# Optimization experiments

Hardware: AMD Instinct MI355X
Metric: run time of the kernel (lower is better)

Reference implementation:

```python
import jax, jax.numpy as jnp
import numpy as np

EPS = 1e-8

def _qparams(x, bits):
    # AsymmetricSignedQParams + GlobalMinMaxObserver: per-tensor min/max,
    # signed range [-2^(b-1), 2^(b-1)-1], asymmetric zero point.
    qmin = -(2 ** (bits - 1))
    qmax = 2 ** (bits - 1) - 1
    mn = jnp.minimum(jnp.min(x), 0.0)
    mx = jnp.maximum(jnp.max(x), 0.0)
    scale = jnp.maximum((mx - mn) / (qmax - qmin), EPS)
    zp = jnp.clip(jnp.round(qmin - mn / scale), qmin, qmax)
    return scale, zp, qmin, qmax

def _fake_quant(x, bits):
    # quantize -> clamp -> dequantize (simulated fixed-point as in float forward)
    scale, zp, qmin, qmax = _qparams(x, bits)
    q = jnp.clip(jnp.round(x / scale) + zp, qmin, qmax)
    return (q - zp) * scale


def setup_inputs() -> dict:
    key = jax.random.key(0)
    k1, k2, k3 = jax.random.split(key, 3)
    B, W, H, D = 8, 1024, 8, 64
    q = jax.random.normal(k1, (B, W, H, D), dtype=jnp.float32)
    k = jax.random.normal(k2, (B, W, H, D), dtype=jnp.float32)
    v = jax.random.normal(k3, (B, W, H, D), dtype=jnp.float32)
    return {"q": q, "k": k, "v": v, "quant_bits": 8}


def reference(q, k, v, quant_bits):
    bits = int(quant_bits)
    d_model = q.shape[-1]
    inv_sqrt_d = 1.0 / np.sqrt(d_model)

    # quantize-dequantize inputs (inputs_{q,k,v}_QParams)
    qf = _fake_quant(q, bits)
    kf = _fake_quant(k, bits)
    vf = _fake_quant(v, bits)

    # matrix_multi_score: quantized QK^T with folded 1/sqrt(d) scale,
    # then requantize output (matrix_multi_score.outputs_QParams)
    scores = jnp.einsum("bqhd,bkhd->bhqk", qf, kf) * inv_sqrt_d
    scores = _fake_quant(scores, bits)

    # SoftmaxLUT: softmax over last dim, result requantized (softmax.outputs_QParams)
    att = jax.nn.softmax(scores, axis=-1)
    att_q = _fake_quant(att, bits)

    # matrix_multi_att: quantized att @ V, requantized output
    context = jnp.einsum("bhqk,bkhd->bqhd", att_q, vf)
    context = _fake_quant(context, bits)

    return context, att_q
```

## Files before the change

kernel.cpp:

```cpp
#include <hip/hip_runtime.h>
#include <cstdint>
#include <cstddef>

#define W  1024
#define NH 8
#define NB 8
#define DH 64
#define BHN (NB*NH)
#define CTX_ELEMS ((size_t)NB*W*NH*DH)
#define NS 64
#define ROWF 512

typedef int v4i __attribute__((ext_vector_type(4)));


__device__ __forceinline__ unsigned enc_f(float f){
  unsigned u = __float_as_uint(f);
  return (u & 0x80000000u) ? ~u : (u | 0x80000000u);
}
__device__ __forceinline__ float dec_f(unsigned k){
  unsigned u = (k & 0x80000000u) ? (k ^ 0x80000000u) : ~k;
  return __uint_as_float(u);
}

__device__ __forceinline__ float fq1(float x, float s, float z, float mn, float mx){
  float t = rintf(x / s) + z;
  t = fminf(fmaxf(t, mn), mx);
  return (t - z) * s;
}
__device__ __forceinline__ int qint_m(float x, float is, float z, float mn, float mx){
  return (int)fminf(fmaxf(rintf(x * is) + z, mn), mx);
}
__device__ __forceinline__ unsigned pack4(int a0, int a1, int a2, int a3){
  return (unsigned)(a0 & 0xff) | ((unsigned)(a1 & 0xff) << 8) |
         ((unsigned)(a2 & 0xff) << 16) | ((unsigned)(a3 & 0xff) << 24);
}

__device__ __forceinline__ unsigned* slot_min(unsigned* s, int t){ return s + (size_t)(2*t)*NS; }
__device__ __forceinline__ unsigned* slot_max(unsigned* s, int t){ return s + (size_t)(2*t+1)*NS; }

__device__ __forceinline__ void blk_minmax_atomic(float lmin, float lmax,
                                                  unsigned* smin, unsigned* smax){
  #pragma unroll
  for (int o = 32; o; o >>= 1){
    lmin = fminf(lmin, __shfl_xor(lmin, o));
    lmax = fmaxf(lmax, __shfl_xor(lmax, o));
  }
  __shared__ float wmn[4], wmx[4];
  int wid = threadIdx.x >> 6, lane = threadIdx.x & 63;
  if (lane == 0){ wmn[wid] = lmin; wmx[wid] = lmax; }
  __syncthreads();
  if (threadIdx.x == 0){
    float a = wmn[0], b = wmx[0];
    for (int w = 1; w < (int)(blockDim.x >> 6); ++w){
      a = fminf(a, wmn[w]); b = fmaxf(b, wmx[w]);
    }
    atomicMin(smin, enc_f(a));
    atomicMax(smax, enc_f(b));
  }
}

__device__ __forceinline__ void blk_iminmax_atomic(int lmin, int lmax, int* gmin, int* gmax){
  #pragma unroll
  for (int o = 32; o; o >>= 1){
    lmin = min(lmin, __shfl_xor(lmin, o));
    lmax = max(lmax, __shfl_xor(lmax, o));
  }
  __shared__ int iwmn[4], iwmx[4];
  int wid = threadIdx.x >> 6, lane = threadIdx.x & 63;
  if (lane == 0){ iwmn[wid] = lmin; iwmx[wid] = lmax; }
  __syncthreads();
  if (threadIdx.x == 0){
    int a = iwmn[0], b = iwmx[0];
    for (int w = 1; w < (int)(blockDim.x >> 6); ++w){
      a = min(a, iwmn[w]); b = max(b, iwmx[w]);
    }
    atomicMin(gmin, a);
    atomicMax(gmax, b);
  }
}

__device__ __forceinline__ void stage_tile(const float* __restrict__ rowptr,
                                           signed char (*S)[80], int* __restrict__ Ssum,
                                           float is, float z, float mn, float mx, int t){
  const int rr = t >> 2, dq = (t & 3) << 4;
  const float* p = rowptr + (size_t)rr * ROWF + dq;
  int part = 0;
  #pragma unroll
  for (int g = 0; g < 4; ++g){
    float4 x = *(const float4*)(p + g * 4);
    int a0 = qint_m(x.x, is, z, mn, mx), a1 = qint_m(x.y, is, z, mn, mx);
    int a2 = qint_m(x.z, is, z, mn, mx), a3 = qint_m(x.w, is, z, mn, mx);
    part += a0 + a1 + a2 + a3;
    *(unsigned*)&S[rr][dq + g*4] = pack4(a0, a1, a2, a3);
  }
  int x1 = part + __shfl_xor(part, 1);
  int tot = x1 + __shfl_xor(x1, 2);
  if ((t & 3) == 0) Ssum[rr] = tot;
}


__global__ void init_slots_kernel(unsigned* __restrict__ slots, int* __restrict__ jmn,
                                  int* __restrict__ jmx){
  for (int i = threadIdx.x; i < 6*2*NS; i += blockDim.x)
    slots[i] = 0x80000000u;
  if (threadIdx.x < NS){
    jmn[threadIdx.x] = 0x7fffffff;
    jmx[threadIdx.x] = (int)0x80000000;
  }
}

__global__ __launch_bounds__(256) void minmax3_kernel(const float* __restrict__ q,
                                                      const float* __restrict__ k,
                                                      const float* __restrict__ v,
                                                      unsigned* __restrict__ slots){
  const float4* p = (const float4*)(blockIdx.y == 0 ? q : (blockIdx.y == 1 ? k : v));
  float lmin = 0.f, lmax = 0.f;
  const int n4 = (int)(CTX_ELEMS / 4);
  for (int i = blockIdx.x * blockDim.x + threadIdx.x; i < n4; i += gridDim.x * blockDim.x){
    float4 x = p[i];
    lmin = fminf(lmin, fminf(fminf(x.x, x.y), fminf(x.z, x.w)));
    lmax = fmaxf(lmax, fmaxf(fmaxf(x.x, x.y), fmaxf(x.z, x.w)));
  }
  const int idx = blockIdx.x & (NS - 1);
  blk_minmax_atomic(lmin, lmax, slot_min(slots, blockIdx.y) + idx, slot_max(slots, blockIdx.y) + idx);
}

__global__ void finalize_kernel(unsigned* __restrict__ slots, int* __restrict__ jmn,
                                int* __restrict__ jmx, float* __restrict__ params,
                                const int* __restrict__ bits_p, int t0, int t1){
  if (threadIdx.x == 0 && blockIdx.x == 0){
    int bits = *bits_p;
    float qmn = -(float)(1 << (bits - 1));
    float qmx = (float)((1 << (bits - 1)) - 1);
    for (int t = t0; t < t1; ++t){
      float mn, mx;
      if (t == 3){
        int em = jmn[0], ex = jmx[0];
        for (int i = 1; i < NS; ++i){ em = min(em, jmn[i]); ex = max(ex, jmx[i]); }
        float cfac = 0.125f * (params[0] * params[4]);
        mn = fminf(cfac * (float)em, 0.0f);
        mx = fmaxf(cfac * (float)ex, 0.0f);
      } else {
        unsigned* pm = slot_min(slots, t);
        unsigned* px = slot_max(slots, t);
        unsigned em = pm[0], ex = px[0];
        for (int i = 1; i < NS; ++i){
          em = (pm[i] < em) ? pm[i] : em;
          ex = (px[i] > ex) ? px[i] : ex;
        }
        mn = dec_f(em); mx = dec_f(ex);
      }
      float sc = fmaxf((mx - mn) / (qmx - qmn), 1e-8f);
      float zp = fminf(fmaxf(rintf(qmn - mn / sc), qmn), qmx);
      params[4*t + 0] = sc; params[4*t + 1] = zp;
      params[4*t + 2] = qmn; params[4*t + 3] = qmx;
    }
  }
}

__global__ __launch_bounds__(256) void pass1_kernel(const float* __restrict__ qg,
                                                    const float* __restrict__ kg,
                                                    const float* __restrict__ params,
                                                    float* __restrict__ stash,
                                                    int* __restrict__ jmn,
                                                    int* __restrict__ jmx){
  __shared__ __align__(16) signed char Qs[64][80], Ks[64][80];
  __shared__ int Sq[64], Sk[64];
  const int it = blockIdx.x, bh = blockIdx.y, b = bh >> 3, h = bh & 7;
  const int i0 = it << 6, t = threadIdx.x;
  const int lane = t & 63, w = t >> 6, lr = lane & 15, lg = lane >> 4;
  const float sq = params[0], zq = params[1], qmn = params[2], qmx = params[3];
  const float sk = params[4], zk = params[5];
  const float isq = 1.0f / sq, isk = 1.0f / sk;
  const int izq = (int)zq, izk = (int)zk, c64 = 64 * izq * izk;

  stage_tile(qg + ((size_t)(b*W + i0) * NH + h) * DH, Qs, Sq, isq, zq, qmn, qmx, t);
  __syncthreads();
  const v4i Bq = *(const v4i*)&Qs[(w << 4) + lr][lg << 4];
  const int sqi = Sq[(w << 4) + lr];

  int gmin = 0x7fffffff, gmax = (int)0x80000000, rmax = (int)0x80000000;
  for (int cc = 0; cc < 16; ++cc){
    __syncthreads();
    stage_tile(kg + ((size_t)(b*W + (cc << 6)) * NH + h) * DH, Ks, Sk, isk, zk, qmn, qmx, t);
    __syncthreads();
    #pragma unroll
    for (int jt = 0; jt < 4; ++jt){
      v4i Ak = *(const v4i*)&Ks[(jt << 4) + lr][lg << 4];
      v4i zz = {0, 0, 0, 0};
      v4i acc = __builtin_amdgcn_mfma_i32_16x16x64_i8(Ak, Bq, zz, 0, 0, 0);
      v4i s4 = *(const v4i*)&Sk[(jt << 4) + (lg << 2)];
      #pragma unroll
      for (int r = 0; r < 4; ++r){
        int J = acc[r] - izq * s4[r] - izk * sqi + c64;
        gmin = min(gmin, J); gmax = max(gmax, J); rmax = max(rmax, J);
      }
    }
  }
  rmax = max(rmax, __shfl_xor(rmax, 16));
  rmax = max(rmax, __shfl_xor(rmax, 32));
  if (lg == 0)
    stash[((size_t)(b*W + i0 + (w << 4) + lr) * NH + h) * DH] = __int_as_float(rmax);
  const int idx = (it + bh * 16) & (NS - 1);
  blk_iminmax_atomic(gmin, gmax, jmn + idx, jmx + idx);
}

__global__ __launch_bounds__(256) void pass2_kernel(const float* __restrict__ qg,
                                                    const float* __restrict__ kg,
                                                    const float* __restrict__ params,
                                                    float* __restrict__ stash,
                                                    unsigned* __restrict__ slots){
  __shared__ __align__(16) signed char Qs[64][80], Ks[64][80];
  __shared__ int Sq[64], Sk[64];
  const int it = blockIdx.x, bh = blockIdx.y, b = bh >> 3, h = bh & 7;
  const int i0 = it << 6, t = threadIdx.x;
  const int lane = t & 63, w = t >> 6, lr = lane & 15, lg = lane >> 4;
  const float sq = params[0], zq = params[1], qmn = params[2], qmx = params[3];
  const float sk = params[4], zk = params[5];
  const float ss = params[12], zs = params[13], smn = params[14], smx = params[15];
  const float isq = 1.0f / sq, isk = 1.0f / sk;
  const int izq = (int)zq, izk = (int)zk, c64 = 64 * izq * izk;
  const float rf = (0.125f * (sq * sk)) / ss;
  const float c2 = ss * 1.4426950408889634f;

  stage_tile(qg + ((size_t)(b*W + i0) * NH + h) * DH, Qs, Sq, isq, zq, qmn, qmx, t);
  __syncthreads();
  const v4i Bq = *(const v4i*)&Qs[(w << 4) + lr][lg << 4];
  const int sqi = Sq[(w << 4) + lr];
  const int irow = (w << 4) + lr;
  int Jm = __float_as_int(stash[((size_t)(b*W + i0 + irow) * NH + h) * DH]);
  const float tmxf = fminf(fmaxf(rintf((float)Jm * rf) + zs, smn), smx);

  float zacc = 0.f;
  for (int cc = 0; cc < 16; ++cc){
    __syncthreads();
    stage_tile(kg + ((size_t)(b*W + (cc << 6)) * NH + h) * DH, Ks, Sk, isk, zk, qmn, qmx, t);
    __syncthreads();
    #pragma unroll
    for (int jt = 0; jt < 4; ++jt){
      v4i Ak = *(const v4i*)&Ks[(jt << 4) + lr][lg << 4];
      v4i zz = {0, 0, 0, 0};
      v4i acc = __builtin_amdgcn_mfma_i32_16x16x64_i8(Ak, Bq, zz, 0, 0, 0);
      v4i s4 = *(const v4i*)&Sk[(jt << 4) + (lg << 2)];
      #pragma unroll
      for (int r = 0; r < 4; ++r){
        int J = acc[r] - izq * s4[r] - izk * sqi + c64;
        float tl = fminf(fmaxf(rintf((float)J * rf) + zs, smn), smx);
        zacc += exp2f((tl - tmxf) * c2);
      }
    }
  }
  zacc += __shfl_xor(zacc, 16);
  zacc += __shfl_xor(zacc, 32);
  if (lg == 0)
    stash[((size_t)(b*W + i0 + irow) * NH + h) * DH + 1] = zacc;
  float ratt = 1.0f / zacc;
  #pragma unroll
  for (int o = 1; o < 16; o <<= 1) ratt = fmaxf(ratt, __shfl_xor(ratt, o));
  if (lane == 0){
    const int idx = ((it << 2) + w + bh * 64) & (NS - 1);
    atomicMax(slot_max(slots, 4) + idx, enc_f(ratt));
  }
}

__global__ __launch_bounds__(256) void pass3_kernel(const float* __restrict__ qg,
                                                    const float* __restrict__ kg,
                                                    const float* __restrict__ vg,
                                                    const float* __restrict__ params,
                                                    float* __restrict__ att,
                                                    float* __restrict__ ctx,
                                                    unsigned* __restrict__ slots){
  __shared__ __align__(16) signed char Qs[64][80], Ks[64][80], Vs[64][80], As[64][80];
  __shared__ int Sq[64], Sk[64];
  __shared__ int RowA[64], ColV[64];
  const int it = blockIdx.x, bh = blockIdx.y, b = bh >> 3, h = bh & 7;
  const int i0 = it << 6, t = threadIdx.x;
  const int lane = t & 63, w = t >> 6, lr = lane & 15, lg = lane >> 4;
  const float sq = params[0], zq = params[1], qmn = params[2], qmx = params[3];
  const float sk = params[4], zk = params[5];
  const float sv = params[8], zv = params[9], vmn = params[10], vmx = params[11];
  const float ss = params[12], zs = params[13], smn = params[14], smx = params[15];
  const float sa = params[16], za = params[17], amn = params[18], amx = params[19];
  const float isq = 1.0f / sq, isk = 1.0f / sk, isv = 1.0f / sv;
  const int izq = (int)zq, izk = (int)zk, c64 = 64 * izq * izk;
  const int iza = (int)za, izv = (int)zv;
  const float rf = (0.125f * (sq * sk)) / ss;
  const float c2 = ss * 1.4426950408889634f;
  const float inv_sa = 1.0f / sa;

  if (t < 64) ColV[t] = 0;
  stage_tile(qg + ((size_t)(b*W + i0) * NH + h) * DH, Qs, Sq, isq, zq, qmn, qmx, t);
  __syncthreads();
  const v4i Bq = *(const v4i*)&Qs[(w << 4) + lr][lg << 4];
  const int sqi = Sq[(w << 4) + lr];
  const int irow = (w << 4) + lr;
  const size_t rbase = ((size_t)(b*W + i0 + irow) * NH + h) * DH;
  int Jm = __float_as_int(ctx[rbase]);
  const float tmxf = fminf(fmaxf(rintf((float)Jm * rf) + zs, smn), smx);
  const float iZ = 1.0f / ctx[rbase + 1];

  const int dq4 = (t & 15) << 2;
  const int kb  = (t >> 4) << 2;
  int cv4[4] = {0, 0, 0, 0};
  int rA = 0;
  v4i accPV[4];
  #pragma unroll
  for (int tj = 0; tj < 4; ++tj){ v4i zz = {0,0,0,0}; accPV[tj] = zz; }

  for (int cc = 0; cc < 16; ++cc){
    __syncthreads();
    stage_tile(kg + ((size_t)(b*W + (cc << 6)) * NH + h) * DH, Ks, Sk, isk, zk, qmn, qmx, t);
    {
      const float* vp = vg + ((size_t)(b*W + (cc << 6) + kb) * NH + h) * DH + dq4;
      float4 x0 = *(const float4*)(vp);
      float4 x1 = *(const float4*)(vp + ROWF);
      float4 x2 = *(const float4*)(vp + 2 * ROWF);
      float4 x3 = *(const float4*)(vp + 3 * ROWF);
      int q00 = qint_m(x0.x, isv, zv, vmn, vmx), q01 = qint_m(x0.y, isv, zv, vmn, vmx),
          q02 = qint_m(x0.z, isv, zv, vmn, vmx), q03 = qint_m(x0.w, isv, zv, vmn, vmx);
      int q10 = qint_m(x1.x, isv, zv, vmn, vmx), q11 = qint_m(x1.y, isv, zv, vmn, vmx),
          q12 = qint_m(x1.z, isv, zv, vmn, vmx), q13 = qint_m(x1.w, isv, zv, vmn, vmx);
      int q20 = qint_m(x2.x, isv, zv, vmn, vmx), q21 = qint_m(x2.y, isv, zv, vmn, vmx),
          q22 = qint_m(x2.z, isv, zv, vmn, vmx), q23 = qint_m(x2.w, isv, zv, vmn, vmx);
      int q30 = qint_m(x3.x, isv, zv, vmn, vmx), q31 = qint_m(x3.y, isv, zv, vmn, vmx),
          q32 = qint_m(x3.z, isv, zv, vmn, vmx), q33 = qint_m(x3.w, isv, zv, vmn, vmx);
      cv4[0] += q00 + q10 + q20 + q30;
      cv4[1] += q01 + q11 + q21 + q31;
      cv4[2] += q02 + q12 + q22 + q32;
      cv4[3] += q03 + q13 + q23 + q33;
      *(unsigned*)&Vs[dq4 + 0][kb] = pack4(q00, q10, q20, q30);
      *(unsigned*)&Vs[dq4 + 1][kb] = pack4(q01, q11, q21, q31);
      *(unsigned*)&Vs[dq4 + 2][kb] = pack4(q02, q12, q22, q32);
      *(unsigned*)&Vs[dq4 + 3][kb] = pack4(q03, q13, q23, q33);
    }
    __syncthreads();
    #pragma unroll
    for (int jt = 0; jt < 4; ++jt){
      v4i Ak = *(const v4i*)&Ks[(jt << 4) + lr][lg << 4];
      v4i zz = {0, 0, 0, 0};
      v4i acc = __builtin_amdgcn_mfma_i32_16x16x64_i8(Ak, Bq, zz, 0, 0, 0);
      v4i s4 = *(const v4i*)&Sk[(jt << 4) + (lg << 2)];
      float4 y;
      int J0 = acc[0] - izq * s4[0] - izk * sqi + c64;
      int J1 = acc[1] - izq * s4[1] - izk * sqi + c64;
      int J2 = acc[2] - izq * s4[2] - izk * sqi + c64;
      int J3 = acc[3] - izq * s4[3] - izk * sqi + c64;
      float tl0 = fminf(fmaxf(rintf((float)J0 * rf) + zs, smn), smx);
      float tl1 = fminf(fmaxf(rintf((float)J1 * rf) + zs, smn), smx);
      float tl2 = fminf(fmaxf(rintf((float)J2 * rf) + zs, smn), smx);
      float tl3 = fminf(fmaxf(rintf((float)J3 * rf) + zs, smn), smx);
      float p0 = exp2f((tl0 - tmxf) * c2) * iZ;
      float p1 = exp2f((tl1 - tmxf) * c2) * iZ;
      float p2 = exp2f((tl2 - tmxf) * c2) * iZ;
      float p3 = exp2f((tl3 - tmxf) * c2) * iZ;
      float a0 = fminf(fmaxf(rintf(p0 * inv_sa) + za, amn), amx);
      float a1 = fminf(fmaxf(rintf(p1 * inv_sa) + za, amn), amx);
      float a2 = fminf(fmaxf(rintf(p2 * inv_sa) + za, amn), amx);
      float a3 = fminf(fmaxf(rintf(p3 * inv_sa) + za, amn), amx);
      y.x = (a0 - za) * sa; y.y = (a1 - za) * sa;
      y.z = (a2 - za) * sa; y.w = (a3 - za) * sa;
      *(float4*)(att + ((size_t)bh << 20) + (size_t)(i0 + irow) * W
                 + (cc << 6) + (jt << 4) + (lg << 2)) = y;
      int q0 = (int)a0, q1 = (int)a1, q2 = (int)a2, q3 = (int)a3;
      rA += q0 + q1 + q2 + q3;
      *(unsigned*)&As[irow][(jt << 4) + (lg << 2)] = pack4(q0, q1, q2, q3);
    }
    __syncthreads();
    {
      v4i A2 = *(const v4i*)&As[(w << 4) + lr][lg << 4];
      #pragma unroll
      for (int tj = 0; tj < 4; ++tj){
        v4i B2 = *(const v4i*)&Vs[(tj << 4) + lr][lg << 4];
        accPV[tj] = __builtin_amdgcn_mfma_i32_16x16x64_i8(A2, B2, accPV[tj], 0, 0, 0);
      }
    }
  }

  rA += __shfl_xor(rA, 16);
  rA += __shfl_xor(rA, 32);
  if (lg == 0) RowA[irow] = rA;
  #pragma unroll
  for (int j = 0; j < 4; ++j) atomicAdd(&ColV[dq4 + j], cv4[j]);
  __syncthreads();

  const float sav = sa * sv;
  float lmin = 0.f, lmax = 0.f;
  #pragma unroll
  for (int tj = 0; tj < 4; ++tj){
    const int d = (tj << 4) + lr;
    #pragma unroll
    for (int r = 0; r < 4; ++r){
      const int i = (w << 4) + (lg << 2) + r;
      int Jv = accPV[tj][r] - iza * ColV[d] - izv * RowA[i] + 1024 * iza * izv;
      float c = sav * (float)Jv;
      lmin = fminf(lmin, c); lmax = fmaxf(lmax, c);
      ctx[(((size_t)(b * W + i0 + i)) * NH + h) * DH + d] = c;
    }
  }
  const int idx = (it + bh * 16) & (NS - 1);
  blk_minmax_atomic(lmin, lmax, slot_min(slots, 5) + idx, slot_max(slots, 5) + idx);
}

__global__ __launch_bounds__(256) void quantctx_kernel(float* __restrict__ ctx,
                                                       const float* __restrict__ params){
  const float s = params[20], z = params[21], mn = params[22], mx = params[23];
  size_t i = (size_t)blockIdx.x * blockDim.x + threadIdx.x;
  float4* p = (float4*)ctx;
  float4 x = p[i];
  x.x = fq1(x.x, s, z, mn, mx);
  x.y = fq1(x.y, s, z, mn, mx);
  x.z = fq1(x.z, s, z, mn, mx);
  x.w = fq1(x.w, s, z, mn, mx);
  p[i] = x;
}


extern "C" void kernel_launch(void* const* d_in, const int* in_sizes, int n_in,
                              void* d_out, int out_size, void* d_ws, size_t ws_size,
                              hipStream_t stream){
  const float* q = (const float*)d_in[0];
  const float* k = (const float*)d_in[1];
  const float* v = (const float*)d_in[2];
  const int* bits = (const int*)d_in[3];
  float* ctx = (float*)d_out;
  float* att = (float*)d_out + CTX_ELEMS;
  unsigned* slots = (unsigned*)d_ws;
  int* jmn = (int*)((char*)d_ws + 3072);
  int* jmx = (int*)((char*)d_ws + 3328);
  float* params = (float*)((char*)d_ws + 3584);

  hipLaunchKernelGGL(init_slots_kernel, dim3(1), dim3(256), 0, stream, slots, jmn, jmx);
  hipLaunchKernelGGL(minmax3_kernel, dim3(512, 3), dim3(256), 0, stream, q, k, v, slots);
  hipLaunchKernelGGL(finalize_kernel, dim3(1), dim3(1), 0, stream, slots, jmn, jmx, params, bits, 0, 3);
  hipLaunchKernelGGL(pass1_kernel, dim3(16, BHN), dim3(256), 0, stream, q, k, params, ctx, jmn, jmx);
  hipLaunchKernelGGL(finalize_kernel, dim3(1), dim3(1), 0, stream, slots, jmn, jmx, params, bits, 3, 4);
  hipLaunchKernelGGL(pass2_kernel, dim3(16, BHN), dim3(256), 0, stream, q, k, params, ctx, slots);
  hipLaunchKernelGGL(finalize_kernel, dim3(1), dim3(1), 0, stream, slots, jmn, jmx, params, bits, 4, 5);
  hipLaunchKernelGGL(pass3_kernel, dim3(16, BHN), dim3(256), 0, stream, q, k, v, params, att, ctx, slots);
  hipLaunchKernelGGL(finalize_kernel, dim3(1), dim3(1), 0, stream, slots, jmn, jmx, params, bits, 5, 6);
  hipLaunchKernelGGL(quantctx_kernel, dim3(4096), dim3(256), 0, stream, ctx, params);
}
```

Before: 238.1 us.

## Cache quantized scores in att buffer and fold finalize into consumer kernels

Pass2 now writes the quantized int8 score codes, packed, into the att output buffer as scratch. Pass3 reads them back instead of restaging Q and K and recomputing the QK^T MFMA, and it drops one barrier. The single-thread finalize kernels are removed: each consumer block recomputes the qparams from the atomic slots itself, which saves four tiny launches but adds redundant per-block reduction loops. This trades the recompute for extra global writes and reads of the packed codes.

New measurement: 281.4 us. +18.2%, slower.

```diff
diff --git a/kernel.cpp b/kernel.cpp
--- a/kernel.cpp
+++ b/kernel.cpp
@@ -10,6 +10,7 @@
 #define CTX_ELEMS ((size_t)NB*W*NH*DH)
 #define NS 64
 #define ROWF 512
+#define L2E 1.4426950408889634f
 
 typedef int v4i __attribute__((ext_vector_type(4)));
 
@@ -38,6 +39,36 @@
 
 __device__ __forceinline__ unsigned* slot_min(unsigned* s, int t){ return s + (size_t)(2*t)*NS; }
 __device__ __forceinline__ unsigned* slot_max(unsigned* s, int t){ return s + (size_t)(2*t+1)*NS; }
+
+struct QP { float s, z; };
+
+__device__ __forceinline__ QP qp_generic(const unsigned* slots, int t, float qmn, float qmx){
+  const unsigned* pm = slots + (size_t)(2*t)*NS;
+  const unsigned* px = pm + NS;
+  unsigned em = pm[0], ex = px[0];
+  for (int i = 1; i < NS; ++i){
+    unsigned a = pm[i], b = px[i];
+    em = (a < em) ? a : em;
+    ex = (b > ex) ? b : ex;
+  }
+  float mn = dec_f(em), mx = dec_f(ex);
+  QP r;
+  r.s = fmaxf((mx - mn) / (qmx - qmn), 1e-8f);
+  r.z = fminf(fmaxf(rintf(qmn - mn / r.s), qmn), qmx);
+  return r;
+}
+__device__ __forceinline__ QP qp_scores(const int* jmn, const int* jmx, float sq, float sk,
+                                        float qmn, float qmx){
+  int em = jmn[0], ex = jmx[0];
+  for (int i = 1; i < NS; ++i){ em = min(em, jmn[i]); ex = max(ex, jmx[i]); }
+  float cfac = 0.125f * (sq * sk);
+  float mn = fminf(cfac * (float)em, 0.0f);
+  float mx = fmaxf(cfac * (float)ex, 0.0f);
+  QP r;
+  r.s = fmaxf((mx - mn) / (qmx - qmn), 1e-8f);
+  r.z = fminf(fmaxf(rintf(qmn - mn / r.s), qmn), qmx);
+  return r;
+}
 
 __device__ __forceinline__ void blk_minmax_atomic(float lmin, float lmax,
                                                   unsigned* smin, unsigned* smax){
@@ -126,56 +157,26 @@
   blk_minmax_atomic(lmin, lmax, slot_min(slots, blockIdx.y) + idx, slot_max(slots, blockIdx.y) + idx);
 }
 
-__global__ void finalize_kernel(unsigned* __restrict__ slots, int* __restrict__ jmn,
-                                int* __restrict__ jmx, float* __restrict__ params,
-                                const int* __restrict__ bits_p, int t0, int t1){
-  if (threadIdx.x == 0 && blockIdx.x == 0){
-    int bits = *bits_p;
-    float qmn = -(float)(1 << (bits - 1));
-    float qmx = (float)((1 << (bits - 1)) - 1);
-    for (int t = t0; t < t1; ++t){
-      float mn, mx;
-      if (t == 3){
-        int em = jmn[0], ex = jmx[0];
-        for (int i = 1; i < NS; ++i){ em = min(em, jmn[i]); ex = max(ex, jmx[i]); }
-        float cfac = 0.125f * (params[0] * params[4]);
-        mn = fminf(cfac * (float)em, 0.0f);
-        mx = fmaxf(cfac * (float)ex, 0.0f);
-      } else {
-        unsigned* pm = slot_min(slots, t);
-        unsigned* px = slot_max(slots, t);
-        unsigned em = pm[0], ex = px[0];
-        for (int i = 1; i < NS; ++i){
-          em = (pm[i] < em) ? pm[i] : em;
-          ex = (px[i] > ex) ? px[i] : ex;
-        }
-        mn = dec_f(em); mx = dec_f(ex);
-      }
-      float sc = fmaxf((mx - mn) / (qmx - qmn), 1e-8f);
-      float zp = fminf(fmaxf(rintf(qmn - mn / sc), qmn), qmx);
-      params[4*t + 0] = sc; params[4*t + 1] = zp;
-      params[4*t + 2] = qmn; params[4*t + 3] = qmx;
-    }
-  }
-}
-
 __global__ __launch_bounds__(256) void pass1_kernel(const float* __restrict__ qg,
                                                     const float* __restrict__ kg,
-                                                    const float* __restrict__ params,
+                                                    const unsigned* __restrict__ slots,
+                                                    const int* __restrict__ bits_p,
                                                     float* __restrict__ stash,
                                                     int* __restrict__ jmn,
                                                     int* __restrict__ jmx){
   __shared__ __align__(16) signed char Qs[64][80], Ks[64][80];
   __shared__ int Sq[64], Sk[64];
+  const int bits = *bits_p;
+  const float qmx = (float)((1 << (bits-1)) - 1), qmn = -(float)(1 << (bits-1));
+  const QP qq = qp_generic(slots, 0, qmn, qmx);
+  const QP kp = qp_generic(slots, 1, qmn, qmx);
   const int it = blockIdx.x, bh = blockIdx.y, b = bh >> 3, h = bh & 7;
   const int i0 = it << 6, t = threadIdx.x;
   const int lane = t & 63, w = t >> 6, lr = lane & 15, lg = lane >> 4;
-  const float sq = params[0], zq = params[1], qmn = params[2], qmx = params[3];
-  const float sk = params[4], zk = params[5];
-  const float isq = 1.0f / sq, isk = 1.0f / sk;
-  const int izq = (int)zq, izk = (int)zk, c64 = 64 * izq * izk;
-
-  stage_tile(qg + ((size_t)(b*W + i0) * NH + h) * DH, Qs, Sq, isq, zq, qmn, qmx, t);
+  const float isq = 1.0f / qq.s, isk = 1.0f / kp.s;
+  const int izq = (int)qq.z, izk = (int)kp.z, c64 = 64 * izq * izk;
+
+  stage_tile(qg + ((size_t)(b*W + i0) * NH + h) * DH, Qs, Sq, isq, qq.z, qmn, qmx, t);
   __syncthreads();
   const v4i Bq = *(const v4i*)&Qs[(w << 4) + lr][lg << 4];
   const int sqi = Sq[(w << 4) + lr];
@@ -183,7 +184,7 @@
   int gmin = 0x7fffffff, gmax = (int)0x80000000, rmax = (int)0x80000000;
   for (int cc = 0; cc < 16; ++cc){
     __syncthreads();
-    stage_tile(kg + ((size_t)(b*W + (cc << 6)) * NH + h) * DH, Ks, Sk, isk, zk, qmn, qmx, t);
+    stage_tile(kg + ((size_t)(b*W + (cc << 6)) * NH + h) * DH, Ks, Sk, isk, kp.z, qmn, qmx, t);
     __syncthreads();
     #pragma unroll
     for (int jt = 0; jt < 4; ++jt){
@@ -208,34 +209,41 @@
 
 __global__ __launch_bounds__(256) void pass2_kernel(const float* __restrict__ qg,
                                                     const float* __restrict__ kg,
-                                                    const float* __restrict__ params,
-                                                    float* __restrict__ stash,
-                                                    unsigned* __restrict__ slots){
+                                                    unsigned* __restrict__ slots,
+                                                    const int* __restrict__ jmn,
+                                                    const int* __restrict__ jmx,
+                                                    const int* __restrict__ bits_p,
+                                                    float* __restrict__ att,
+                                                    float* __restrict__ stash){
   __shared__ __align__(16) signed char Qs[64][80], Ks[64][80];
   __shared__ int Sq[64], Sk[64];
+  const int bits = *bits_p;
+  const float qmx = (float)((1 << (bits-1)) - 1), qmn = -(float)(1 << (bits-1));
+  const QP qq = qp_generic(slots, 0, qmn, qmx);
+  const QP kp = qp_generic(slots, 1, qmn, qmx);
+  const QP sp = qp_scores(jmn, jmx, qq.s, kp.s, qmn, qmx);
   const int it = blockIdx.x, bh = blockIdx.y, b = bh >> 3, h = bh & 7;
   const int i0 = it << 6, t = threadIdx.x;
   const int lane = t & 63, w = t >> 6, lr = lane & 15, lg = lane >> 4;
-  const float sq = params[0], zq = params[1], qmn = params[2], qmx = params[3];
-  const float sk = params[4], zk = params[5];
-  const float ss = params[12], zs = params[13], smn = params[14], smx = params[15];
-  const float isq = 1.0f / sq, isk = 1.0f / sk;
-  const int izq = (int)zq, izk = (int)zk, c64 = 64 * izq * izk;
-  const float rf = (0.125f * (sq * sk)) / ss;
-  const float c2 = ss * 1.4426950408889634f;
-
-  stage_tile(qg + ((size_t)(b*W + i0) * NH + h) * DH, Qs, Sq, isq, zq, qmn, qmx, t);
+  const float isq = 1.0f / qq.s, isk = 1.0f / kp.s;
+  const int izq = (int)qq.z, izk = (int)kp.z, c64 = 64 * izq * izk;
+  const float rf = (0.125f * (qq.s * kp.s)) / sp.s;
+  const float c2 = sp.s * L2E;
+  const float zs = sp.z;
+
+  stage_tile(qg + ((size_t)(b*W + i0) * NH + h) * DH, Qs, Sq, isq, qq.z, qmn, qmx, t);
   __syncthreads();
   const v4i Bq = *(const v4i*)&Qs[(w << 4) + lr][lg << 4];
   const int sqi = Sq[(w << 4) + lr];
   const int irow = (w << 4) + lr;
   int Jm = __float_as_int(stash[((size_t)(b*W + i0 + irow) * NH + h) * DH]);
-  const float tmxf = fminf(fmaxf(rintf((float)Jm * rf) + zs, smn), smx);
+  const float tmxf = fminf(fmaxf(rintf((float)Jm * rf) + zs, qmn), qmx);
+  const size_t rowbase = ((size_t)bh << 20) + ((size_t)(i0 + irow) << 10);
 
   float zacc = 0.f;
   for (int cc = 0; cc < 16; ++cc){
     __syncthreads();
-    stage_tile(kg + ((size_t)(b*W + (cc << 6)) * NH + h) * DH, Ks, Sk, isk, zk, qmn, qmx, t);
+    stage_tile(kg + ((size_t)(b*W + (cc << 6)) * NH + h) * DH, Ks, Sk, isk, kp.z, qmn, qmx, t);
     __syncthreads();
     #pragma unroll
     for (int jt = 0; jt < 4; ++jt){
@@ -243,12 +251,20 @@
       v4i zz = {0, 0, 0, 0};
       v4i acc = __builtin_amdgcn_mfma_i32_16x16x64_i8(Ak, Bq, zz, 0, 0, 0);
       v4i s4 = *(const v4i*)&Sk[(jt << 4) + (lg << 2)];
-      #pragma unroll
-      for (int r = 0; r < 4; ++r){
-        int J = acc[r] - izq * s4[r] - izk * sqi + c64;
-        float tl = fminf(fmaxf(rintf((float)J * rf) + zs, smn), smx);
-        zacc += exp2f((tl - tmxf) * c2);
-      }
+      int J0 = acc[0] - izq * s4[0] - izk * sqi + c64;
+      int J1 = acc[1] - izq * s4[1] - izk * sqi + c64;
+      int J2 = acc[2] - izq * s4[2] - izk * sqi + c64;
+      int J3 = acc[3] - izq * s4[3] - izk * sqi + c64;
+      float tl0 = fminf(fmaxf(rintf((float)J0 * rf) + zs, qmn), qmx);
+      float tl1 = fminf(fmaxf(rintf((float)J1 * rf) + zs, qmn), qmx);
+      float tl2 = fminf(fmaxf(rintf((float)J2 * rf) + zs, qmn), qmx);
+      float tl3 = fminf(fmaxf(rintf((float)J3 * rf) + zs, qmn), qmx);
+      zacc += exp2f((tl0 - tmxf) * c2);
+      zacc += exp2f((tl1 - tmxf) * c2);
+      zacc += exp2f((tl2 - tmxf) * c2);
+      zacc += exp2f((tl3 - tmxf) * c2);
+      att[rowbase + (cc << 6) + (lg << 2) + jt] =
+        __uint_as_float(pack4((int)tl0, (int)tl1, (int)tl2, (int)tl3));
     }
   }
   zacc += __shfl_xor(zacc, 16);
@@ -264,41 +280,38 @@
   }
 }
 
-__global__ __launch_bounds__(256) void pass3_kernel(const float* __restrict__ qg,
-                                                    const float* __restrict__ kg,
-                                                    const float* __restrict__ vg,
-                                                    const float* __restrict__ params,
+__global__ __launch_bounds__(256) void pass3_kernel(const float* __restrict__ vg,
                                                     float* __restrict__ att,
                                                     float* __restrict__ ctx,
-                                                    unsigned* __restrict__ slots){
-  __shared__ __align__(16) signed char Qs[64][80], Ks[64][80], Vs[64][80], As[64][80];
-  __shared__ int Sq[64], Sk[64];
+                                                    unsigned* __restrict__ slots,
+                                                    const int* __restrict__ jmn,
+                                                    const int* __restrict__ jmx,
+                                                    const int* __restrict__ bits_p){
+  __shared__ __align__(16) signed char Vs[64][80], As[64][80];
   __shared__ int RowA[64], ColV[64];
+  const int bits = *bits_p;
+  const float qmx = (float)((1 << (bits-1)) - 1), qmn = -(float)(1 << (bits-1));
+  const QP qq = qp_generic(slots, 0, qmn, qmx);
+  const QP kp = qp_generic(slots, 1, qmn, qmx);
+  const QP sp = qp_scores(jmn, jmx, qq.s, kp.s, qmn, qmx);
+  const QP vp = qp_generic(slots, 2, qmn, qmx);
+  const QP ap = qp_generic(slots, 4, qmn, qmx);
   const int it = blockIdx.x, bh = blockIdx.y, b = bh >> 3, h = bh & 7;
   const int i0 = it << 6, t = threadIdx.x;
   const int lane = t & 63, w = t >> 6, lr = lane & 15, lg = lane >> 4;
-  const float sq = params[0], zq = params[1], qmn = params[2], qmx = params[3];
-  const float sk = params[4], zk = params[5];
-  const float sv = params[8], zv = params[9], vmn = params[10], vmx = params[11];
-  const float ss = params[12], zs = params[13], smn = params[14], smx = params[15];
-  const float sa = params[16], za = params[17], amn = params[18], amx = params[19];
-  const float isq = 1.0f / sq, isk = 1.0f / sk, isv = 1.0f / sv;
-  const int izq = (int)zq, izk = (int)zk, c64 = 64 * izq * izk;
+  const float rf = (0.125f * (qq.s * kp.s)) / sp.s;
+  const float c2 = sp.s * L2E, zs = sp.z;
+  const float sa = ap.s, za = ap.z, inv_sa = 1.0f / sa;
+  const float sv = vp.s, zv = vp.z, isv = 1.0f / sv;
   const int iza = (int)za, izv = (int)zv;
-  const float rf = (0.125f * (sq * sk)) / ss;
-  const float c2 = ss * 1.4426950408889634f;
-  const float inv_sa = 1.0f / sa;
 
   if (t < 64) ColV[t] = 0;
-  stage_tile(qg + ((size_t)(b*W + i0) * NH + h) * DH, Qs, Sq, isq, zq, qmn, qmx, t);
-  __syncthreads();
-  const v4i Bq = *(const v4i*)&Qs[(w << 4) + lr][lg << 4];
-  const int sqi = Sq[(w << 4) + lr];
   const int irow = (w << 4) + lr;
   const size_t rbase = ((size_t)(b*W + i0 + irow) * NH + h) * DH;
   int Jm = __float_as_int(ctx[rbase]);
-  const float tmxf = fminf(fmaxf(rintf((float)Jm * rf) + zs, smn), smx);
+  const float tmxf = fminf(fmaxf(rintf((float)Jm * rf) + zs, qmn), qmx);
   const float iZ = 1.0f / ctx[rbase + 1];
+  const size_t rowbase = ((size_t)bh << 20) + ((size_t)(i0 + irow) << 10);
 
   const int dq4 = (t & 15) << 2;
   const int kb  = (t >> 4) << 2;
@@ -310,21 +323,20 @@
 
   for (int cc = 0; cc < 16; ++cc){
     __syncthreads();
-    stage_tile(kg + ((size_t)(b*W + (cc << 6)) * NH + h) * DH, Ks, Sk, isk, zk, qmn, qmx, t);
     {
-      const float* vp = vg + ((size_t)(b*W + (cc << 6) + kb) * NH + h) * DH + dq4;
-      float4 x0 = *(const float4*)(vp);
-      float4 x1 = *(const float4*)(vp + ROWF);
-      float4 x2 = *(const float4*)(vp + 2 * ROWF);
-      float4 x3 = *(const float4*)(vp + 3 * ROWF);
-      int q00 = qint_m(x0.x, isv, zv, vmn, vmx), q01 = qint_m(x0.y, isv, zv, vmn, vmx),
-          q02 = qint_m(x0.z, isv, zv, vmn, vmx), q03 = qint_m(x0.w, isv, zv, vmn, vmx);
-      int q10 = qint_m(x1.x, isv, zv, vmn, vmx), q11 = qint_m(x1.y, isv, zv, vmn, vmx),
-          q12 = qint_m(x1.z, isv, zv, vmn, vmx), q13 = qint_m(x1.w, isv, zv, vmn, vmx);
-      int q20 = qint_m(x2.x, isv, zv, vmn, vmx), q21 = qint_m(x2.y, isv, zv, vmn, vmx),
-          q22 = qint_m(x2.z, isv, zv, vmn, vmx), q23 = qint_m(x2.w, isv, zv, vmn, vmx);
-      int q30 = qint_m(x3.x, isv, zv, vmn, vmx), q31 = qint_m(x3.y, isv, zv, vmn, vmx),
-          q32 = qint_m(x3.z, isv, zv, vmn, vmx), q33 = qint_m(x3.w, isv, zv, vmn, vmx);
+      const float* vp_ = vg + ((size_t)(b*W + (cc << 6) + kb) * NH + h) * DH + dq4;
+      float4 x0 = *(const float4*)(vp_);
+      float4 x1 = *(const float4*)(vp_ + ROWF);
+      float4 x2 = *(const float4*)(vp_ + 2 * ROWF);
+      float4 x3 = *(const float4*)(vp_ + 3 * ROWF);
+      int q00 = qint_m(x0.x, isv, zv, qmn, qmx), q01 = qint_m(x0.y, isv, zv, qmn, qmx),
+          q02 = qint_m(x0.z, isv, zv, qmn, qmx), q03 = qint_m(x0.w, isv, zv, qmn, qmx);
+      int q10 = qint_m(x1.x, isv, zv, qmn, qmx), q11 = qint_m(x1.y, isv, zv, qmn, qmx),
+          q12 = qint_m(x1.z, isv, zv, qmn, qmx), q13 = qint_m(x1.w, isv, zv, qmn, qmx);
+      int q20 = qint_m(x2.x, isv, zv, qmn, qmx), q21 = qint_m(x2.y, isv, zv, qmn, qmx),
+          q22 = qint_m(x2.z, isv, zv, qmn, qmx), q23 = qint_m(x2.w, isv, zv, qmn, qmx);
+      int q30 = qint_m(x3.x, isv, zv, qmn, qmx), q31 = qint_m(x3.y, isv, zv, qmn, qmx),
+          q32 = qint_m(x3.z, isv, zv, qmn, qmx), q33 = qint_m(x3.w, isv, zv, qmn, qmx);
       cv4[0] += q00 + q10 + q20 + q30;
       cv4[1] += q01 + q11 + q21 + q31;
       cv4[2] += q02 + q12 + q22 + q32;
@@ -335,38 +347,34 @@
       *(unsigned*)&Vs[dq4 + 3][kb] = pack4(q03, q13, q23, q33);
     }
     __syncthreads();
+
+    const size_t cb = rowbase + ((size_t)cc << 6);
+    float4 tf = *(const float4*)(att + cb + (lg << 2));
+    unsigned uu[4] = { __float_as_uint(tf.x), __float_as_uint(tf.y),
+                       __float_as_uint(tf.z), __float_as_uint(tf.w) };
     #pragma unroll
     for (int jt = 0; jt < 4; ++jt){
-      v4i Ak = *(const v4i*)&Ks[(jt << 4) + lr][lg << 4];
-      v4i zz = {0, 0, 0, 0};
-      v4i acc = __builtin_amdgcn_mfma_i32_16x16x64_i8(Ak, Bq, zz, 0, 0, 0);
-      v4i s4 = *(const v4i*)&Sk[(jt << 4) + (lg << 2)];
+      unsigned u = uu[jt];
+      float t0 = (float)(int)(signed char)(u & 0xff);
+      float t1 = (float)(int)(signed char)((u >> 8) & 0xff);
+      float t2 = (float)(int)(signed char)((u >> 16) & 0xff);
+      float t3 = (float)(int)(signed char)((u >> 24) & 0xff);
+      float p0 = exp2f((t0 - tmxf) * c2) * iZ;
+      float p1 = exp2f((t1 - tmxf) * c2) * iZ;
+      float p2 = exp2f((t2 - tmxf) * c2) * iZ;
+      float p3 = exp2f((t3 - tmxf) * c2) * iZ;
+      float a0 = fminf(fmaxf(rintf(p0 * inv_sa) + za, qmn), qmx);
+      float a1 = fminf(fmaxf(rintf(p1 * inv_sa) + za, qmn), qmx);
+      float a2 = fminf(fmaxf(rintf(p2 * inv_sa) + za, qmn), qmx);
+      float a3 = fminf(fmaxf(rintf(p3 * inv_sa) + za, qmn), qmx);
       float4 y;
-      int J0 = acc[0] - izq * s4[0] - izk * sqi + c64;
-      int J1 = acc[1] - izq * s4[1] - izk * sqi + c64;
-      int J2 = acc[2] - izq * s4[2] - izk * sqi + c64;
-      int J3 = acc[3] - izq * s4[3] - izk * sqi + c64;
-      float tl0 = fminf(fmaxf(rintf((float)J0 * rf) + zs, smn), smx);
-      float tl1 = fminf(fmaxf(rintf((float)J1 * rf) + zs, smn), smx);
-      float tl2 = fminf(fmaxf(rintf((float)J2 * rf) + zs, smn), smx);
-      float tl3 = fminf(fmaxf(rintf((float)J3 * rf) + zs, smn), smx);
-      float p0 = exp2f((tl0 - tmxf) * c2) * iZ;
-      float p1 = exp2f((tl1 - tmxf) * c2) * iZ;
-      float p2 = exp2f((tl2 - tmxf) * c2) * iZ;
-      float p3 = exp2f((tl3 - tmxf) * c2) * iZ;
-      float a0 = fminf(fmaxf(rintf(p0 * inv_sa) + za, amn), amx);
-      float a1 = fminf(fmaxf(rintf(p1 * inv_sa) + za, amn), amx);
-      float a2 = fminf(fmaxf(rintf(p2 * inv_sa) + za, amn), amx);
-      float a3 = fminf(fmaxf(rintf(p3 * inv_sa) + za, amn), amx);
       y.x = (a0 - za) * sa; y.y = (a1 - za) * sa;
       y.z = (a2 - za) * sa; y.w = (a3 - za) * sa;
-      *(float4*)(att + ((size_t)bh << 20) + (size_t)(i0 + irow) * W
-                 + (cc << 6) + (jt << 4) + (lg << 2)) = y;
+      *(float4*)(att + cb + (jt << 4) + (lg << 2)) = y;
       int q0 = (int)a0, q1 = (int)a1, q2 = (int)a2, q3 = (int)a3;
       rA += q0 + q1 + q2 + q3;
       *(unsigned*)&As[irow][(jt << 4) + (lg << 2)] = pack4(q0, q1, q2, q3);
     }
-    __syncthreads();
     {
       v4i A2 = *(const v4i*)&As[(w << 4) + lr][lg << 4];
       #pragma unroll
@@ -403,15 +411,18 @@
 }
 
 __global__ __launch_bounds__(256) void quantctx_kernel(float* __restrict__ ctx,
-                                                       const float* __restrict__ params){
-  const float s = params[20], z = params[21], mn = params[22], mx = params[23];
+                                                       const unsigned* __restrict__ slots,
+                                                       const int* __restrict__ bits_p){
+  const int bits = *bits_p;
+  const float qmx = (float)((1 << (bits-1)) - 1), qmn = -(float)(1 << (bits-1));
+  const QP cp = qp_generic(slots, 5, qmn, qmx);
   size_t i = (size_t)blockIdx.x * blockDim.x + threadIdx.x;
   float4* p = (float4*)ctx;
   float4 x = p[i];
-  x.x = fq1(x.x, s, z, mn, mx);
-  x.y = fq1(x.y, s, z, mn, mx);
-  x.z = fq1(x.z, s, z, mn, mx);
-  x.w = fq1(x.w, s, z, mn, mx);
+  x.x = fq1(x.x, cp.s, cp.z, qmn, qmx);
+  x.y = fq1(x.y, cp.s, cp.z, qmn, qmx);
+  x.z = fq1(x.z, cp.s, cp.z, qmn, qmx);
+  x.w = fq1(x.w, cp.s, cp.z, qmn, qmx);
   p[i] = x;
 }
 
@@ -428,16 +439,11 @@
   unsigned* slots = (unsigned*)d_ws;
   int* jmn = (int*)((char*)d_ws + 3072);
   int* jmx = (int*)((char*)d_ws + 3328);
-  float* params = (float*)((char*)d_ws + 3584);
 
   hipLaunchKernelGGL(init_slots_kernel, dim3(1), dim3(256), 0, stream, slots, jmn, jmx);
   hipLaunchKernelGGL(minmax3_kernel, dim3(512, 3), dim3(256), 0, stream, q, k, v, slots);
-  hipLaunchKernelGGL(finalize_kernel, dim3(1), dim3(1), 0, stream, slots, jmn, jmx, params, bits, 0, 3);
-  hipLaunchKernelGGL(pass1_kernel, dim3(16, BHN), dim3(256), 0, stream, q, k, params, ctx, jmn, jmx);
-  hipLaunchKernelGGL(finalize_kernel, dim3(1), dim3(1), 0, stream, slots, jmn, jmx, params, bits, 3, 4);
-  hipLaunchKernelGGL(pass2_kernel, dim3(16, BHN), dim3(256), 0, stream, q, k, params, ctx, slots);
-  hipLaunchKernelGGL(finalize_kernel, dim3(1), dim3(1), 0, stream, slots, jmn, jmx, params, bits, 4, 5);
-  hipLaunchKernelGGL(pass3_kernel, dim3(16, BHN), dim3(256), 0, stream, q, k, v, params, att, ctx, slots);
-  hipLaunchKernelGGL(finalize_kernel, dim3(1), dim3(1), 0, stream, slots, jmn, jmx, params, bits, 5, 6);
-  hipLaunchKernelGGL(quantctx_kernel, dim3(4096), dim3(256), 0, stream, ctx, params);
-}
+  hipLaunchKernelGGL(pass1_kernel, dim3(16, BHN), dim3(256), 0, stream, q, k, slots, bits, ctx, jmn, jmx);
+  hipLaunchKernelGGL(pass2_kernel, dim3(16, BHN), dim3(256), 0, stream, q, k, slots, jmn, jmx, bits, att, ctx);
+  hipLaunchKernelGGL(pass3_kernel, dim3(16, BHN), dim3(256), 0, stream, v, att, ctx, slots, jmn, jmx, bits);
+  hipLaunchKernelGGL(quantctx_kernel, dim3(4096), dim3(256), 0, stream, ctx, slots, bits);
+}
```
